# Kernel optimization log

Measured on AMD Instinct MI355X. Metric: run time of the kernel, lower is better.

Reference implementation:

```python
import jax, jax.numpy as jnp
import numpy as np

B, T, D, H, E = 4, 2048, 1024, 2048, 8

def setup_inputs() -> dict:
    key = jax.random.key(0)
    ks = jax.random.split(key, 7)
    s_in = 1.0 / np.sqrt(D)
    s_hid = 1.0 / np.sqrt(H)
    return {
        "x": jax.random.normal(ks[0], (B, T, D), dtype=jnp.float32),
        "Wg": jax.random.uniform(ks[1], (D, E), jnp.float32, -s_in, s_in),
        "bg": jax.random.uniform(ks[2], (E,), jnp.float32, -s_in, s_in),
        "W1": jax.random.uniform(ks[3], (E, D, H), jnp.float32, -s_in, s_in),
        "b1": jax.random.uniform(ks[4], (E, H), jnp.float32, -s_in, s_in),
        "W2": jax.random.uniform(ks[5], (E, H, D), jnp.float32, -s_hid, s_hid),
        "b2": jax.random.uniform(ks[6], (E, D), jnp.float32, -s_hid, s_hid),
    }

def reference(x, Wg, bg, W1, b1, W2, b2):
    # gating: [B,T,E]
    gate = jax.nn.softmax(jnp.einsum('btd,de->bte', x, Wg) + bg, axis=-1)
    # all experts densely: hidden [B,T,E,H]
    h = jax.nn.relu(jnp.einsum('btd,edh->bteh', x, W1) + b1)
    # expert outputs [B,T,E,D]
    eo = jnp.einsum('bteh,ehd->bted', h, W2) + b2
    # softmax-weighted sum over experts -> [B,T,D]
    return jnp.einsum('bte,bted->btd', gate, eo)
```

## Files before the change

### kernel.cpp

```cpp
#include <hip/hip_runtime.h>
#include <hip/hip_bf16.h>
#include <stdint.h>


typedef __bf16 bf16_t;
typedef bf16_t bf16x8 __attribute__((ext_vector_type(8)));
typedef bf16_t bf16x4 __attribute__((ext_vector_type(4)));
typedef float  f32x4  __attribute__((ext_vector_type(4)));

#define Ddim 1024
#define Hdim 2048
#define Edim 8
#define Mdim 8192

__device__ __forceinline__ void async16(const void* g, const void* l) {
  __builtin_amdgcn_global_load_lds(
      (const __attribute__((address_space(1))) void*)(uintptr_t)g,
      (__attribute__((address_space(3))) void*)(uint32_t)(uintptr_t)l,
      16, 0, 0);
}

#define MFMA(a, b, c) __builtin_amdgcn_mfma_f32_16x16x32_bf16((a), (b), (c), 0, 0, 0)

#define WAIT_VM0() do {                                    \
    asm volatile("s_waitcnt vmcnt(0)" ::: "memory");       \
    __builtin_amdgcn_sched_barrier(0);                     \
  } while (0)

__global__ void gating_kernel(const float* __restrict__ x,
                              const float* __restrict__ Wg,
                              const float* __restrict__ bg,
                              float* __restrict__ gate) {
  const int lane = threadIdx.x & 63;
  const int wid  = threadIdx.x >> 6;
  const int t    = blockIdx.x * 4 + wid;
  const float* xr = x + (size_t)t * Ddim;
  float acc[8] = {0.f,0.f,0.f,0.f,0.f,0.f,0.f,0.f};
  for (int i = lane; i < Ddim; i += 64) {
    float xv = xr[i];
    f32x4 a = *(const f32x4*)(Wg + (size_t)i * 8);
    f32x4 b = *(const f32x4*)(Wg + (size_t)i * 8 + 4);
    acc[0] += xv * a[0]; acc[1] += xv * a[1];
    acc[2] += xv * a[2]; acc[3] += xv * a[3];
    acc[4] += xv * b[0]; acc[5] += xv * b[1];
    acc[6] += xv * b[2]; acc[7] += xv * b[3];
  }
  #pragma unroll
  for (int e = 0; e < 8; ++e) {
    #pragma unroll
    for (int off = 32; off; off >>= 1)
      acc[e] += __shfl_xor(acc[e], off, 64);
  }
  if (lane == 0) {
    float l[8], mx = -1e30f;
    #pragma unroll
    for (int e = 0; e < 8; ++e) { l[e] = acc[e] + bg[e]; mx = fmaxf(mx, l[e]); }
    float s = 0.f;
    #pragma unroll
    for (int e = 0; e < 8; ++e) { l[e] = __expf(l[e] - mx); s += l[e]; }
    float inv = 1.f / s;
    #pragma unroll
    for (int e = 0; e < 8; ++e) gate[(size_t)t * 8 + e] = l[e] * inv;
  }
}

__global__ void cvt_x(const float* __restrict__ a, bf16_t* __restrict__ o) {
  const size_t i = ((size_t)blockIdx.x * 256 + threadIdx.x) * 8;
  f32x4 v0 = *(const f32x4*)(a + i);
  f32x4 v1 = *(const f32x4*)(a + i + 4);
  bf16x8 b;
  b[0]=(bf16_t)v0[0]; b[1]=(bf16_t)v0[1]; b[2]=(bf16_t)v0[2]; b[3]=(bf16_t)v0[3];
  b[4]=(bf16_t)v1[0]; b[5]=(bf16_t)v1[1]; b[6]=(bf16_t)v1[2]; b[7]=(bf16_t)v1[3];
  *(bf16x8*)(o + i) = b;
}

__global__ void transpose_f32_bf16(const float* __restrict__ src,
                                   bf16_t* __restrict__ dst, int R, int C) {
  __shared__ bf16_t tile[32][33];
  const size_t zo = (size_t)blockIdx.z * (size_t)R * C;
  src += zo; dst += zo;
  const int r0 = blockIdx.y * 32, c0 = blockIdx.x * 32;
  const int tr = threadIdx.x >> 3;
  const int tc = (threadIdx.x & 7) * 4;
  f32x4 v = *(const f32x4*)(src + (size_t)(r0 + tr) * C + c0 + tc);
  tile[tr][tc+0] = (bf16_t)v[0]; tile[tr][tc+1] = (bf16_t)v[1];
  tile[tr][tc+2] = (bf16_t)v[2]; tile[tr][tc+3] = (bf16_t)v[3];
  __syncthreads();
  bf16x4 o;
  o[0] = tile[tc+0][tr]; o[1] = tile[tc+1][tr];
  o[2] = tile[tc+2][tr]; o[3] = tile[tc+3][tr];
  *(bf16x4*)(dst + (size_t)(c0 + tr) * R + r0 + tc) = o;
}

__launch_bounds__(512, 2)
__global__ void gemm1_kernel(const bf16_t* __restrict__ A,
                             const bf16_t* __restrict__ W1tAll,
                             const float*  __restrict__ gate,
                             const float*  __restrict__ b1,
                             bf16_t* __restrict__ hgAll,
                             int e0) {
  __shared__ alignas(16) bf16_t sA[2][256 * 64];
  __shared__ alignas(16) bf16_t sB[2][256 * 64];

  const int tid  = threadIdx.x;
  const int lane = tid & 63;
  const int wid  = tid >> 6;
  const int wm   = wid >> 2, wn = wid & 3;
  const int lrow = lane & 15, quad = lane >> 4;
  const int sb   = quad ^ (lrow & 7);

  const int z = blockIdx.z;
  const int e = e0 + z;
  const bf16_t* Bt = W1tAll + (size_t)z * Hdim * Ddim;
  bf16_t* hg = hgAll + (size_t)z * (size_t)Mdim * Hdim;
  const float* bias = b1 + (size_t)e * Hdim;

  const int bid = blockIdx.y * 8 + blockIdx.x;
  const int xcd = bid & 7, loc = bid >> 3;
  const int tileM = (xcd * 4 + (loc >> 3)) * 256;
  const int tileN = (loc & 7) * 256;

  const int trow = tid >> 3;
  const int tsw  = ((tid & 7) ^ (trow & 7)) << 4;
  const int ldst = tid << 4;
  const size_t SA = (size_t)64 * Ddim * 2;

  const char* a0 = (const char*)(A  + (size_t)(tileM + trow) * Ddim) + tsw;
  const char* b0 = (const char*)(Bt + (size_t)(tileN + trow) * Ddim) + tsw;
  char* curA = (char*)&sA[0][0]; char* nxtA = (char*)&sA[1][0];
  char* curB = (char*)&sB[0][0]; char* nxtB = (char*)&sB[1][0];

  async16(a0,          curA + 0 * 8192 + ldst);
  async16(a0 + SA,     curA + 1 * 8192 + ldst);
  async16(a0 + 2 * SA, curA + 2 * 8192 + ldst);
  async16(a0 + 3 * SA, curA + 3 * 8192 + ldst);
  async16(b0,          curB + 0 * 8192 + ldst);
  async16(b0 + SA,     curB + 1 * 8192 + ldst);
  async16(b0 + 2 * SA, curB + 2 * 8192 + ldst);
  async16(b0 + 3 * SA, curB + 3 * 8192 + ldst);
  a0 += 128; b0 += 128;
  WAIT_VM0();
  __builtin_amdgcn_s_barrier();

  f32x4 acc[8][4] = {};
  const int offA0 = (wm * 128 + lrow) * 128 + sb * 16;
  const int offA1 = (wm * 128 + lrow) * 128 + (sb ^ 4) * 16;
  const int offB0 = (wn * 64  + lrow) * 128 + sb * 16;
  const int offB1 = (wn * 64  + lrow) * 128 + (sb ^ 4) * 16;

  #pragma unroll 1
  for (int kk = 0; kk < Ddim / 64; ++kk) {
    const bool notlast = (kk + 1 < Ddim / 64);
    __builtin_amdgcn_sched_barrier(0);
    if (notlast) {
      async16(a0,          nxtA + 0 * 8192 + ldst);
      async16(a0 + SA,     nxtA + 1 * 8192 + ldst);
      async16(a0 + 2 * SA, nxtA + 2 * 8192 + ldst);
      async16(a0 + 3 * SA, nxtA + 3 * 8192 + ldst);
      async16(b0,          nxtB + 0 * 8192 + ldst);
      async16(b0 + SA,     nxtB + 1 * 8192 + ldst);
      async16(b0 + 2 * SA, nxtB + 2 * 8192 + ldst);
      async16(b0 + 3 * SA, nxtB + 3 * 8192 + ldst);
    }
    bf16x8 afr[8][2], bfr[4][2];
    #pragma unroll
    for (int i = 0; i < 8; ++i) {
      afr[i][0] = *(const bf16x8*)(curA + offA0 + i * 2048);
      afr[i][1] = *(const bf16x8*)(curA + offA1 + i * 2048);
    }
    #pragma unroll
    for (int j = 0; j < 4; ++j) {
      bfr[j][0] = *(const bf16x8*)(curB + offB0 + j * 2048);
      bfr[j][1] = *(const bf16x8*)(curB + offB1 + j * 2048);
    }
    __builtin_amdgcn_s_setprio(1);
    #pragma unroll
    for (int i = 0; i < 8; ++i)
      #pragma unroll
      for (int j = 0; j < 4; ++j) {
        acc[i][j] = MFMA(afr[i][0], bfr[j][0], acc[i][j]);
        acc[i][j] = MFMA(afr[i][1], bfr[j][1], acc[i][j]);
      }
    __builtin_amdgcn_s_setprio(0);
    WAIT_VM0();
    __builtin_amdgcn_s_barrier();
    a0 += 128; b0 += 128;
    char* t;
    t = curA; curA = nxtA; nxtA = t;
    t = curB; curB = nxtB; nxtB = t;
  }

  const int col0 = tileN + wn * 64 + lrow;
  float bcol[4];
  #pragma unroll
  for (int j = 0; j < 4; ++j) bcol[j] = bias[col0 + j * 16];
  #pragma unroll
  for (int i = 0; i < 8; ++i) {
    #pragma unroll
    for (int r = 0; r < 4; ++r) {
      const int row = tileM + wm * 128 + i * 16 + quad * 4 + r;
      const float g = gate[(size_t)row * 8 + e];
      #pragma unroll
      for (int j = 0; j < 4; ++j) {
        float v = acc[i][j][r] + bcol[j];
        v = fmaxf(v, 0.f) * g;
        hg[(size_t)row * Hdim + col0 + j * 16] = (bf16_t)v;
      }
    }
  }
}

template <int G, bool FIRST>
__launch_bounds__(512, 2)
__global__ void gemm2_kernel(const bf16_t* __restrict__ hgAll,
                             const bf16_t* __restrict__ W2tAll,
                             const float*  __restrict__ gate,
                             const float*  __restrict__ b2,
                             float* __restrict__ out,
                             int e0) {
  __shared__ alignas(16) bf16_t sA[2][256 * 64];
  __shared__ alignas(16) bf16_t sB[2][128 * 64];

  const int tid  = threadIdx.x;
  const int lane = tid & 63;
  const int wid  = tid >> 6;
  const int wm   = wid >> 1, wn = wid & 1;
  const int lrow = lane & 15, quad = lane >> 4;
  const int sb   = quad ^ (lrow & 7);

  const int bid = blockIdx.y * 8 + blockIdx.x;
  const int xcd = bid & 7, loc = bid >> 3;
  const int tileM = (xcd * 4 + (loc >> 3)) * 256;
  const int tileN = (loc & 7) * 128;

  const int trow = tid >> 3;
  const int tsw  = ((tid & 7) ^ (trow & 7)) << 4;
  const int ldst = tid << 4;
  const size_t S = (size_t)64 * Hdim * 2;

  const char* a0 = (const char*)(hgAll  + (size_t)(tileM + trow) * Hdim) + tsw;
  const char* b0 = (const char*)(W2tAll + (size_t)(tileN + trow) * Hdim) + tsw;
  char* curA = (char*)&sA[0][0]; char* nxtA = (char*)&sA[1][0];
  char* curB = (char*)&sB[0][0]; char* nxtB = (char*)&sB[1][0];

  async16(a0,         curA + 0 * 8192 + ldst);
  async16(a0 + S,     curA + 1 * 8192 + ldst);
  async16(a0 + 2 * S, curA + 2 * 8192 + ldst);
  async16(a0 + 3 * S, curA + 3 * 8192 + ldst);
  async16(b0,         curB + 0 * 8192 + ldst);
  async16(b0 + S,     curB + 1 * 8192 + ldst);
  a0 += 128; b0 += 128;
  WAIT_VM0();
  __builtin_amdgcn_s_barrier();

  f32x4 acc[4][4] = {};
  const int offA0 = (wm * 64 + lrow) * 128 + sb * 16;
  const int offA1 = (wm * 64 + lrow) * 128 + (sb ^ 4) * 16;
  const int offB0 = (wn * 64 + lrow) * 128 + sb * 16;
  const int offB1 = (wn * 64 + lrow) * 128 + (sb ^ 4) * 16;

  const int NKT = G * (Hdim / 64);
  #pragma unroll 1
  for (int kk = 0; kk < NKT; ++kk) {
    const bool notlast = (kk + 1 < NKT);
    __builtin_amdgcn_sched_barrier(0);
    if (notlast && (((kk + 1) & 31) == 0)) {
      const int gn = (kk + 1) >> 5;
      a0 = (const char*)(hgAll  + (size_t)gn * Mdim * Hdim
                         + (size_t)(tileM + trow) * Hdim) + tsw;
      b0 = (const char*)(W2tAll + (size_t)gn * Ddim * Hdim
                         + (size_t)(tileN + trow) * Hdim) + tsw;
    }
    if (notlast) {
      async16(a0,         nxtA + 0 * 8192 + ldst);
      async16(a0 + S,     nxtA + 1 * 8192 + ldst);
      async16(a0 + 2 * S, nxtA + 2 * 8192 + ldst);
      async16(a0 + 3 * S, nxtA + 3 * 8192 + ldst);
      async16(b0,         nxtB + 0 * 8192 + ldst);
      async16(b0 + S,     nxtB + 1 * 8192 + ldst);
    }
    bf16x8 afr[4][2], bfr[4][2];
    #pragma unroll
    for (int i = 0; i < 4; ++i) {
      afr[i][0] = *(const bf16x8*)(curA + offA0 + i * 2048);
      afr[i][1] = *(const bf16x8*)(curA + offA1 + i * 2048);
    }
    #pragma unroll
    for (int j = 0; j < 4; ++j) {
      bfr[j][0] = *(const bf16x8*)(curB + offB0 + j * 2048);
      bfr[j][1] = *(const bf16x8*)(curB + offB1 + j * 2048);
    }
    __builtin_amdgcn_s_setprio(1);
    #pragma unroll
    for (int i = 0; i < 4; ++i)
      #pragma unroll
      for (int j = 0; j < 4; ++j) {
        acc[i][j] = MFMA(afr[i][0], bfr[j][0], acc[i][j]);
        acc[i][j] = MFMA(afr[i][1], bfr[j][1], acc[i][j]);
      }
    __builtin_amdgcn_s_setprio(0);
    WAIT_VM0();
    __builtin_amdgcn_s_barrier();
    a0 += 128; b0 += 128;
    char* t;
    t = curA; curA = nxtA; nxtA = t;
    t = curB; curB = nxtB; nxtB = t;
  }

  const int col0 = tileN + wn * 64 + lrow;
  float b2c[4][G];
  #pragma unroll
  for (int j = 0; j < 4; ++j)
    #pragma unroll
    for (int g = 0; g < G; ++g)
      b2c[j][g] = b2[(size_t)(e0 + g) * Ddim + col0 + j * 16];

  #pragma unroll
  for (int i = 0; i < 4; ++i) {
    #pragma unroll
    for (int r = 0; r < 4; ++r) {
      const int row = tileM + wm * 64 + i * 16 + quad * 4 + r;
      const float* gr = gate + (size_t)row * 8 + e0;
      float gv[G];
      #pragma unroll
      for (int g = 0; g < G; ++g) gv[g] = gr[g];
      #pragma unroll
      for (int j = 0; j < 4; ++j) {
        float v = acc[i][j][r];
        #pragma unroll
        for (int g = 0; g < G; ++g) v += gv[g] * b2c[j][g];
        if (FIRST) out[(size_t)row * Ddim + col0 + j * 16] = v;
        else       out[(size_t)row * Ddim + col0 + j * 16] += v;
      }
    }
  }
}

extern "C" void kernel_launch(void* const* d_in, const int* in_sizes, int n_in,
                              void* d_out, int out_size, void* d_ws, size_t ws_size,
                              hipStream_t stream) {
  const float* x  = (const float*)d_in[0];
  const float* Wg = (const float*)d_in[1];
  const float* bg = (const float*)d_in[2];
  const float* W1 = (const float*)d_in[3];
  const float* b1 = (const float*)d_in[4];
  const float* W2 = (const float*)d_in[5];
  const float* b2 = (const float*)d_in[6];
  float* out = (float*)d_out;

  int G = 1;
  if      (ws_size >= (size_t)(17 + 40 * 8) << 20) G = 8;
  else if (ws_size >= (size_t)(17 + 40 * 4) << 20) G = 4;
  else if (ws_size >= (size_t)(17 + 40 * 2) << 20) G = 2;

  char* ws = (char*)d_ws;
  float*  gate = (float*)ws;
  bf16_t* xb   = (bf16_t*)(ws + (1u << 20));
  bf16_t* W1t  = (bf16_t*)(ws + (17u << 20));
  bf16_t* W2t  = (bf16_t*)(ws + ((size_t)(17 + 4 * G) << 20));
  bf16_t* hg   = (bf16_t*)(ws + ((size_t)(17 + 8 * G) << 20));

  gating_kernel<<<Mdim / 4, 256, 0, stream>>>(x, Wg, bg, gate);
  cvt_x<<<(Mdim * Ddim) / (256 * 8), 256, 0, stream>>>(x, xb);

  const int nGroups = Edim / G;
  for (int gi = 0; gi < nGroups; ++gi) {
    const int e0 = gi * G;
    transpose_f32_bf16<<<dim3(Hdim / 32, Ddim / 32, G), 256, 0, stream>>>(
        W1 + (size_t)e0 * Ddim * Hdim, W1t, Ddim, Hdim);
    transpose_f32_bf16<<<dim3(Ddim / 32, Hdim / 32, G), 256, 0, stream>>>(
        W2 + (size_t)e0 * Hdim * Ddim, W2t, Hdim, Ddim);

    gemm1_kernel<<<dim3(Hdim / 256, Mdim / 256, G), 512, 0, stream>>>(
        xb, W1t, gate, b1, hg, e0);

    const dim3 g2(Ddim / 128, Mdim / 256);
    const bool first = (gi == 0);
    if (G == 8)      gemm2_kernel<8, true ><<<g2, 512, 0, stream>>>(hg, W2t, gate, b2, out, e0);
    else if (G == 4) {
      if (first)     gemm2_kernel<4, true ><<<g2, 512, 0, stream>>>(hg, W2t, gate, b2, out, e0);
      else           gemm2_kernel<4, false><<<g2, 512, 0, stream>>>(hg, W2t, gate, b2, out, e0);
    } else if (G == 2) {
      if (first)     gemm2_kernel<2, true ><<<g2, 512, 0, stream>>>(hg, W2t, gate, b2, out, e0);
      else           gemm2_kernel<2, false><<<g2, 512, 0, stream>>>(hg, W2t, gate, b2, out, e0);
    } else {
      if (first)     gemm2_kernel<1, true ><<<g2, 512, 0, stream>>>(hg, W2t, gate, b2, out, e0);
      else           gemm2_kernel<1, false><<<g2, 512, 0, stream>>>(hg, W2t, gate, b2, out, e0);
    }
  }
}
```

Measured before the change: 720.8 us.

## Fuse gating with bf16 cast, merge weight transposes, stream A fragments in GEMMs

Folds the x-to-bf16 conversion into the gating kernel so x is read once, and merges the W1 and W2 transposes into a single launch indexed by blockIdx.y. In both GEMM inner loops, A fragments are now loaded one row-block ahead of the MFMAs instead of all up front, which cuts register pressure and overlaps LDS reads with matrix math. The fused cast writes bf16 with scalar 2-byte stores, which coalesce less well than the old 16-byte vector stores.

```diff
diff --git a/kernel.cpp b/kernel.cpp
--- a/kernel.cpp
+++ b/kernel.cpp
@@ -27,17 +27,20 @@
     __builtin_amdgcn_sched_barrier(0);                     \
   } while (0)
 
-__global__ void gating_kernel(const float* __restrict__ x,
-                              const float* __restrict__ Wg,
-                              const float* __restrict__ bg,
-                              float* __restrict__ gate) {
+__global__ void gating_cvt_kernel(const float* __restrict__ x,
+                                  const float* __restrict__ Wg,
+                                  const float* __restrict__ bg,
+                                  float* __restrict__ gate,
+                                  bf16_t* __restrict__ xb) {
   const int lane = threadIdx.x & 63;
   const int wid  = threadIdx.x >> 6;
   const int t    = blockIdx.x * 4 + wid;
   const float* xr = x + (size_t)t * Ddim;
+  bf16_t* xbr = xb + (size_t)t * Ddim;
   float acc[8] = {0.f,0.f,0.f,0.f,0.f,0.f,0.f,0.f};
   for (int i = lane; i < Ddim; i += 64) {
     float xv = xr[i];
+    xbr[i] = (bf16_t)xv;
     f32x4 a = *(const f32x4*)(Wg + (size_t)i * 8);
     f32x4 b = *(const f32x4*)(Wg + (size_t)i * 8 + 4);
     acc[0] += xv * a[0]; acc[1] += xv * a[1];
@@ -64,22 +67,26 @@
   }
 }
 
-__global__ void cvt_x(const float* __restrict__ a, bf16_t* __restrict__ o) {
-  const size_t i = ((size_t)blockIdx.x * 256 + threadIdx.x) * 8;
-  f32x4 v0 = *(const f32x4*)(a + i);
-  f32x4 v1 = *(const f32x4*)(a + i + 4);
-  bf16x8 b;
-  b[0]=(bf16_t)v0[0]; b[1]=(bf16_t)v0[1]; b[2]=(bf16_t)v0[2]; b[3]=(bf16_t)v0[3];
-  b[4]=(bf16_t)v1[0]; b[5]=(bf16_t)v1[1]; b[6]=(bf16_t)v1[2]; b[7]=(bf16_t)v1[3];
-  *(bf16x8*)(o + i) = b;
-}
-
-__global__ void transpose_f32_bf16(const float* __restrict__ src,
-                                   bf16_t* __restrict__ dst, int R, int C) {
+__global__ void transpose_both(const float* __restrict__ W1s,
+                               const float* __restrict__ W2s,
+                               bf16_t* __restrict__ W1t,
+                               bf16_t* __restrict__ W2t) {
   __shared__ bf16_t tile[32][33];
-  const size_t zo = (size_t)blockIdx.z * (size_t)R * C;
-  src += zo; dst += zo;
-  const int r0 = blockIdx.y * 32, c0 = blockIdx.x * 32;
+  const int G = gridDim.y >> 1;
+  const int z = blockIdx.y;
+  const float* src; bf16_t* dst; int C, bx, by;
+  if (z < G) {
+    src = W1s + (size_t)z * Ddim * Hdim;
+    dst = W1t + (size_t)z * Ddim * Hdim;
+    C = Hdim; bx = blockIdx.x & 63; by = blockIdx.x >> 6;
+  } else {
+    const int e = z - G;
+    src = W2s + (size_t)e * Ddim * Hdim;
+    dst = W2t + (size_t)e * Ddim * Hdim;
+    C = Ddim; bx = blockIdx.x & 31; by = blockIdx.x >> 5;
+  }
+  const int R = (z < G) ? Ddim : Hdim;
+  const int r0 = by * 32, c0 = bx * 32;
   const int tr = threadIdx.x >> 3;
   const int tc = (threadIdx.x & 7) * 4;
   f32x4 v = *(const f32x4*)(src + (size_t)(r0 + tr) * C + c0 + tc);
@@ -162,26 +169,33 @@
       async16(b0 + 2 * SA, nxtB + 2 * 8192 + ldst);
       async16(b0 + 3 * SA, nxtB + 3 * 8192 + ldst);
     }
-    bf16x8 afr[8][2], bfr[4][2];
-    #pragma unroll
-    for (int i = 0; i < 8; ++i) {
-      afr[i][0] = *(const bf16x8*)(curA + offA0 + i * 2048);
-      afr[i][1] = *(const bf16x8*)(curA + offA1 + i * 2048);
-    }
+    __builtin_amdgcn_sched_barrier(0);
+
+    bf16x8 bfr[4][2];
     #pragma unroll
     for (int j = 0; j < 4; ++j) {
       bfr[j][0] = *(const bf16x8*)(curB + offB0 + j * 2048);
       bfr[j][1] = *(const bf16x8*)(curB + offB1 + j * 2048);
     }
+    bf16x8 ca0 = *(const bf16x8*)(curA + offA0);
+    bf16x8 ca1 = *(const bf16x8*)(curA + offA1);
     __builtin_amdgcn_s_setprio(1);
     #pragma unroll
-    for (int i = 0; i < 8; ++i)
+    for (int i = 0; i < 8; ++i) {
+      bf16x8 na0, na1;
+      if (i < 7) {
+        na0 = *(const bf16x8*)(curA + offA0 + (i + 1) * 2048);
+        na1 = *(const bf16x8*)(curA + offA1 + (i + 1) * 2048);
+      }
       #pragma unroll
       for (int j = 0; j < 4; ++j) {
-        acc[i][j] = MFMA(afr[i][0], bfr[j][0], acc[i][j]);
-        acc[i][j] = MFMA(afr[i][1], bfr[j][1], acc[i][j]);
-      }
+        acc[i][j] = MFMA(ca0, bfr[j][0], acc[i][j]);
+        acc[i][j] = MFMA(ca1, bfr[j][1], acc[i][j]);
+      }
+      if (i < 7) { ca0 = na0; ca1 = na1; }
+    }
     __builtin_amdgcn_s_setprio(0);
+
     WAIT_VM0();
     __builtin_amdgcn_s_barrier();
     a0 += 128; b0 += 128;
@@ -279,25 +293,31 @@
       async16(b0,         nxtB + 0 * 8192 + ldst);
       async16(b0 + S,     nxtB + 1 * 8192 + ldst);
     }
-    bf16x8 afr[4][2], bfr[4][2];
-    #pragma unroll
-    for (int i = 0; i < 4; ++i) {
-      afr[i][0] = *(const bf16x8*)(curA + offA0 + i * 2048);
-      afr[i][1] = *(const bf16x8*)(curA + offA1 + i * 2048);
-    }
+    __builtin_amdgcn_sched_barrier(0);
+
+    bf16x8 bfr[4][2];
     #pragma unroll
     for (int j = 0; j < 4; ++j) {
       bfr[j][0] = *(const bf16x8*)(curB + offB0 + j * 2048);
       bfr[j][1] = *(const bf16x8*)(curB + offB1 + j * 2048);
     }
+    bf16x8 ca0 = *(const bf16x8*)(curA + offA0);
+    bf16x8 ca1 = *(const bf16x8*)(curA + offA1);
     __builtin_amdgcn_s_setprio(1);
     #pragma unroll
-    for (int i = 0; i < 4; ++i)
+    for (int i = 0; i < 4; ++i) {
+      bf16x8 na0, na1;
+      if (i < 3) {
+        na0 = *(const bf16x8*)(curA + offA0 + (i + 1) * 2048);
+        na1 = *(const bf16x8*)(curA + offA1 + (i + 1) * 2048);
+      }
       #pragma unroll
       for (int j = 0; j < 4; ++j) {
-        acc[i][j] = MFMA(afr[i][0], bfr[j][0], acc[i][j]);
-        acc[i][j] = MFMA(afr[i][1], bfr[j][1], acc[i][j]);
-      }
+        acc[i][j] = MFMA(ca0, bfr[j][0], acc[i][j]);
+        acc[i][j] = MFMA(ca1, bfr[j][1], acc[i][j]);
+      }
+      if (i < 3) { ca0 = na0; ca1 = na1; }
+    }
     __builtin_amdgcn_s_setprio(0);
     WAIT_VM0();
     __builtin_amdgcn_s_barrier();
@@ -360,16 +380,13 @@
   bf16_t* W2t  = (bf16_t*)(ws + ((size_t)(17 + 4 * G) << 20));
   bf16_t* hg   = (bf16_t*)(ws + ((size_t)(17 + 8 * G) << 20));
 
-  gating_kernel<<<Mdim / 4, 256, 0, stream>>>(x, Wg, bg, gate);
-  cvt_x<<<(Mdim * Ddim) / (256 * 8), 256, 0, stream>>>(x, xb);
+  gating_cvt_kernel<<<Mdim / 4, 256, 0, stream>>>(x, Wg, bg, gate, xb);
 
   const int nGroups = Edim / G;
   for (int gi = 0; gi < nGroups; ++gi) {
     const int e0 = gi * G;
-    transpose_f32_bf16<<<dim3(Hdim / 32, Ddim / 32, G), 256, 0, stream>>>(
-        W1 + (size_t)e0 * Ddim * Hdim, W1t, Ddim, Hdim);
-    transpose_f32_bf16<<<dim3(Ddim / 32, Hdim / 32, G), 256, 0, stream>>>(
-        W2 + (size_t)e0 * Hdim * Ddim, W2t, Hdim, Ddim);
+    transpose_both<<<dim3(2048, 2 * G), 256, 0, stream>>>(
+        W1 + (size_t)e0 * Ddim * Hdim, W2 + (size_t)e0 * Hdim * Ddim, W1t, W2t);
 
     gemm1_kernel<<<dim3(Hdim / 256, Mdim / 256, G), 512, 0, stream>>>(
         xb, W1t, gate, b1, hg, e0);
```

Measured after the change: 695.6 us. 1.04x faster.
